# Kernel optimization log

Hardware: AMD Instinct MI355X
Metric: run time of the kernel (lower is better)

The kernel has to match this reference:

```python
import jax, jax.numpy as jnp
import numpy as np

N = 512      # nodes
E = 512      # edges = nb-graph nodes
M = 16384    # nb-graph edges
FIN = 64     # in_node_nf
HID = 128    # hidden_nf
D = 32       # VTV_coord_nf (positional-encoding width)


def _silu(v):
    return v * jax.nn.sigmoid(v)


def _mlp(v, w1, b1, w2, b2):
    # 2-layer MLP with SiLU (matches MLP(in, out, [hidden]))
    return _silu(v @ w1 + b1) @ w2 + b2


def setup_inputs() -> dict:
    key = jax.random.key(0)
    ks = jax.random.split(key, 32)

    def lin(k, i, o, scale=None):
        s = (1.0 / np.sqrt(i)) if scale is None else scale
        return jax.random.normal(k, (i, o), dtype=jnp.float32) * jnp.float32(s)

    inp = {}
    inp['h'] = jax.random.normal(ks[0], (N, FIN), dtype=jnp.float32)
    inp['x'] = jax.random.normal(ks[1], (N, 3), dtype=jnp.float32)
    inp['edges'] = jax.random.randint(ks[2], (2, E), 0, N)
    inp['nb_edge'] = jax.random.randint(ks[3], (2, M), 0, E)
    inp['edge_attr'] = jax.random.normal(ks[4], (E, 4), dtype=jnp.float32)
    inp['nb_num_nodes'] = E  # python int (static)
    # edge_encoder: MLP(2*FIN -> HID -> FIN)
    inp['ew1'] = lin(ks[5], 2 * FIN, HID); inp['eb1'] = jnp.zeros((HID,), jnp.float32)
    inp['ew2'] = lin(ks[6], HID, FIN);     inp['eb2'] = jnp.zeros((FIN,), jnp.float32)
    # PPGN mlp1 / mlp2: MLP(D+FIN -> HID -> FIN)
    inp['p1w1'] = lin(ks[7], D + FIN, HID); inp['p1b1'] = jnp.zeros((HID,), jnp.float32)
    inp['p1w2'] = lin(ks[8], HID, FIN);     inp['p1b2'] = jnp.zeros((FIN,), jnp.float32)
    inp['p2w1'] = lin(ks[9], D + FIN, HID); inp['p2b1'] = jnp.zeros((HID,), jnp.float32)
    inp['p2w2'] = lin(ks[10], HID, FIN);    inp['p2b2'] = jnp.zeros((FIN,), jnp.float32)
    # PPGN output mlp: MLP(D+FIN+FIN -> HID -> FIN) on concat(skip, matmul)
    inp['p3w1'] = lin(ks[11], D + 2 * FIN, HID); inp['p3b1'] = jnp.zeros((HID,), jnp.float32)
    inp['p3w2'] = lin(ks[12], HID, FIN);         inp['p3b2'] = jnp.zeros((FIN,), jnp.float32)
    # IGN 2->1: linear over 5 basis ops
    inp['ign_w'] = lin(ks[13], 5 * FIN, FIN); inp['ign_b'] = jnp.zeros((FIN,), jnp.float32)
    # coord_mlp: Linear(FIN,HID), SiLU, Linear(HID,1,bias=False) with tiny init
    inp['cw1'] = lin(ks[14], FIN, HID); inp['cb1'] = jnp.zeros((HID,), jnp.float32)
    inp['cw2'] = lin(ks[15], HID, 1, scale=0.001)
    # node_dec: MLP(FIN -> HID -> FIN)
    inp['ndw1'] = lin(ks[16], FIN, HID); inp['ndb1'] = jnp.zeros((HID,), jnp.float32)
    inp['ndw2'] = lin(ks[17], HID, FIN); inp['ndb2'] = jnp.zeros((FIN,), jnp.float32)
    return inp


def reference(h, x, edges, nb_edge, edge_attr, nb_num_nodes,
              ew1, eb1, ew2, eb2,
              p1w1, p1b1, p1w2, p1b2,
              p2w1, p2b1, p2w2, p2b2,
              p3w1, p3b1, p3w2, p3b2,
              ign_w, ign_b,
              cw1, cb1, cw2,
              ndw1, ndb1, ndw2, ndb2):
    rows, cols = edges[0], edges[1]
    coord_diff = x[rows] - x[cols]                      # [E,3]
    nbr, nbc = nb_edge[0], nb_edge[1]
    # VTV: inner product of the two relative-position vectors of paired edges
    vtv = jnp.sum(coord_diff[nbr] * coord_diff[nbc], axis=-1)   # [M]
    # sinusoidal positional encoding, a_scale = D/2
    half = D // 2
    div_term = jnp.exp(jnp.log(jnp.float32(10000.0)) * (2.0 * jnp.arange(half, dtype=jnp.float32) / D))
    ang = vtv[:, None] * jnp.float32(D / 2) / div_term          # [M, D/2]
    pe = jnp.stack([jnp.sin(ang), jnp.cos(ang)], axis=-1).reshape(vtv.shape[0], D)
    # node-pair features per original edge
    efn = _mlp(jnp.concatenate([h[rows], h[cols]], axis=1), ew1, eb1, ew2, eb2)  # [E,FIN]
    nb_feat = jnp.concatenate([pe, efn[nbr] * efn[nbc]], axis=1)                 # [M, D+FIN]
    # densify nb-graph 2-tensor and run PPGN block
    En = nb_num_nodes
    T = jnp.zeros((En, En, nb_feat.shape[1]), dtype=nb_feat.dtype).at[nbr, nbc].add(nb_feat)
    m1 = _mlp(T, p1w1, p1b1, p1w2, p1b2)                 # [En,En,FIN]
    m2 = _mlp(T, p2w1, p2b1, p2w2, p2b2)
    mult = jnp.einsum('ikf,kjf->ijf', m1, m2)            # feature-wise matmul
    Tout = _mlp(jnp.concatenate([T, mult], axis=-1), p3w1, p3b1, p3w2, p3b2)
    # IGN 2->1: diag, row-sum, col-sum, total-sum, trace (broadcast)
    idx = jnp.arange(En)
    diag = Tout[idx, idx]                                # [En,FIN]
    rowsum = Tout.sum(axis=1)
    colsum = Tout.sum(axis=0)
    tot = jnp.broadcast_to(Tout.sum(axis=(0, 1)), diag.shape)
    tr = jnp.broadcast_to(diag.sum(axis=0), diag.shape)
    nb_t1 = jnp.concatenate([diag, rowsum, colsum, tot, tr], axis=1) @ ign_w + ign_b  # [En,FIN]
    # coord update: weighted coord_diff, segment-mean over source node
    w = _silu(nb_t1 @ cw1 + cb1) @ cw2                   # [E,1]
    trans = coord_diff * w
    Nn = x.shape[0]
    seg = jax.ops.segment_sum(trans, rows, num_segments=Nn)
    cnt = jax.ops.segment_sum(jnp.ones((rows.shape[0], 1), trans.dtype), rows, num_segments=Nn)
    x_new = x + seg / jnp.clip(cnt, 1.0)
    # node update: scatter_add edge features then residual MLP
    nb_t0 = jax.ops.segment_sum(nb_t1, rows, num_segments=Nn)
    h_new = h + _mlp(nb_t0, ndw1, ndb1, ndw2, ndb2)
    return (h_new, x_new, edge_attr)
```

## Files before the change

### kernel.cpp

```cpp
#include <hip/hip_runtime.h>
#include <hip/hip_bf16.h>

#define NN   512
#define EE   512
#define MM   16384

typedef float v4f __attribute__((ext_vector_type(4)));
typedef short short8v __attribute__((ext_vector_type(8)));

__device__ __forceinline__ float silu_f(float v) { return v / (1.0f + __expf(-v)); }
__device__ __forceinline__ float silu_fast(float v) {
  return v * __builtin_amdgcn_rcpf(1.0f + __expf(-v));
}

__global__ __launch_bounds__(128) void k_front(
    const float* __restrict__ h, const float* __restrict__ x,
    const int* __restrict__ edges, const int* __restrict__ nb_edge,
    const float* __restrict__ ew1, const float* __restrict__ eb1,
    const float* __restrict__ ew2, const float* __restrict__ eb2,
    const float* __restrict__ p1b1, const float* __restrict__ p1w2, const float* __restrict__ p1b2,
    const float* __restrict__ p2b1, const float* __restrict__ p2w2, const float* __restrict__ p2b2,
    const float* __restrict__ p3w1,
    float* __restrict__ coord_diff, float* __restrict__ efn,
    float* __restrict__ c1, float* __restrict__ c2,
    __hip_bfloat16* __restrict__ Wt, int* __restrict__ slotmap) {
  __shared__ float sm[256];
  int b = blockIdx.x, t = threadIdx.x;
  if (b < 512) {
    int r = edges[b], c = edges[EE + b];
    if (t < 3) coord_diff[b * 3 + t] = x[r * 3 + t] - x[c * 3 + t];
    if (t < 64) { sm[t] = h[r * 64 + t]; sm[64 + t] = h[c * 64 + t]; }
    __syncthreads();
    float acc = eb1[t];
    for (int k = 0; k < 128; ++k) acc += sm[k] * ew1[k * 128 + t];
    sm[128 + t] = silu_f(acc);
    __syncthreads();
    if (t < 64) {
      float o = eb2[t];
      for (int k = 0; k < 128; ++k) o += sm[128 + k] * ew2[k * 64 + t];
      efn[b * 64 + t] = o;
    }
  } else if (b == 512) {
    sm[t] = silu_f(p1b1[t]); sm[128 + t] = silu_f(p2b1[t]);
    __syncthreads();
    if (t < 64) {
      float a1 = p1b2[t], a2 = p2b2[t];
      for (int k = 0; k < 128; ++k) { a1 += sm[k] * p1w2[k * 64 + t]; a2 += sm[128 + k] * p2w2[k * 64 + t]; }
      c1[t] = a1; c2[t] = a2;
    }
  } else if (b < 577) {
    int e = (b - 513) * 128 + t;
    int hh = e >> 6, f = e & 63;
    Wt[hh * 64 + f] = __float2bfloat16(p3w1[(96 + f) * 128 + hh]);
  } else {
    int m = (b - 577) * 128 + t;
    int cell = nb_edge[m] * 512 + nb_edge[MM + m];
    atomicCAS(&slotmap[cell], -1, -2);
  }
}

__global__ __launch_bounds__(256) void k_compact(int* __restrict__ slotmap,
                                                 int* __restrict__ slotmapT,
                                                 int* __restrict__ cells,
                                                 int* __restrict__ nC) {
  int cell = blockIdx.x * 256 + threadIdx.x;
  if (slotmap[cell] != -2) return;
  int s = atomicAdd(nC, 1);
  slotmap[cell] = s;
  slotmapT[(cell & 511) * 512 + (cell >> 9)] = s;
  cells[s] = cell;
}

__global__ __launch_bounds__(192) void k_scatterT(
    const int* __restrict__ nb_edge, const int* __restrict__ slotmap,
    const float* __restrict__ coord_diff, const float* __restrict__ efn,
    float* __restrict__ Tc) {
  int t = threadIdx.x;
  int sub = (t >= 96) ? 1 : 0;
  int c = t - sub * 96;
  int m = blockIdx.x * 2 + sub;
  int a = nb_edge[m], b = nb_edge[MM + m];
  int s = slotmap[a * 512 + b];
  float val;
  if (c < 32) {
    float vtv = coord_diff[a * 3 + 0] * coord_diff[b * 3 + 0]
              + coord_diff[a * 3 + 1] * coord_diff[b * 3 + 1]
              + coord_diff[a * 3 + 2] * coord_diff[b * 3 + 2];
    int i = c >> 1;
    float ang = vtv * 16.0f * __expf(-0.57564627324851143f * (float)i);
    val = (c & 1) ? cosf(ang) : sinf(ang);
  } else {
    int f = c - 32;
    val = efn[a * 64 + f] * efn[b * 64 + f];
  }
  atomicAdd(&Tc[s * 96 + c], val);
}

__global__ __launch_bounds__(128) void k_mlp96b(
    const int* __restrict__ cells, const int* __restrict__ nC, const float* __restrict__ Tc,
    const float* __restrict__ w11, const float* __restrict__ b11,
    const float* __restrict__ w12, const float* __restrict__ b12,
    const float* __restrict__ w21, const float* __restrict__ b21,
    const float* __restrict__ w22, const float* __restrict__ b22,
    const float* __restrict__ c1, const float* __restrict__ c2,
    const float* __restrict__ p3w1,
    __hip_bfloat16* __restrict__ Dc1, __hip_bfloat16* __restrict__ Dc2,
    float* __restrict__ A, float* __restrict__ B,
    float* __restrict__ TWc) {
  __shared__ float xsT[96 * 16];
  __shared__ float hid[16][128];
  __shared__ int cl[16];
  int t = threadIdx.x;
  int nc = *nC;
  int s0 = blockIdx.x * 16;
  if (s0 >= nc) return;
  for (int e = t; e < 1536; e += 128) xsT[(e % 96) * 16 + e / 96] = Tc[s0 * 96 + e];
  if (t < 16) cl[t] = (s0 + t < nc) ? cells[s0 + t] : 0;
  __syncthreads();
  float tw[16], a1[16], a2[16];
#pragma unroll
  for (int c = 0; c < 16; ++c) { tw[c] = 0.f; a1[c] = b11[t]; a2[c] = b21[t]; }
  for (int k = 0; k < 96; ++k) {
    float wt = p3w1[k * 128 + t];
    float w1v = w11[k * 128 + t];
    float w2v = w21[k * 128 + t];
    const float4* xr = (const float4*)&xsT[k * 16];
    float4 x0 = xr[0], x1 = xr[1], x2 = xr[2], x3 = xr[3];
    float xv[16] = {x0.x, x0.y, x0.z, x0.w, x1.x, x1.y, x1.z, x1.w,
                    x2.x, x2.y, x2.z, x2.w, x3.x, x3.y, x3.z, x3.w};
#pragma unroll
    for (int c = 0; c < 16; ++c) {
      tw[c] += xv[c] * wt; a1[c] += xv[c] * w1v; a2[c] += xv[c] * w2v;
    }
  }
#pragma unroll
  for (int c = 0; c < 16; ++c) {
    if (s0 + c < nc) TWc[(s0 + c) * 128 + t] = tw[c];
    hid[c][t] = silu_f(a1[c]);
  }
  __syncthreads();
  {
    int hh = t & 63, cq = t >> 6;
    float o[8];
#pragma unroll
    for (int cc = 0; cc < 8; ++cc) o[cc] = b12[hh];
    for (int k = 0; k < 128; ++k) {
      float w = w12[k * 64 + hh];
#pragma unroll
      for (int cc = 0; cc < 8; ++cc) o[cc] += hid[cq * 8 + cc][k] * w;
    }
#pragma unroll
    for (int cc = 0; cc < 8; ++cc) {
      int c = cq * 8 + cc;
      if (s0 + c < nc) {
        float d = o[cc] - c1[hh];
        int cell = cl[c];
        int ai = cell >> 9;
        atomicAdd(&A[ai * 64 + hh], d);
        Dc1[(s0 + c) * 64 + hh] = __float2bfloat16(d);
      }
    }
  }
  __syncthreads();
#pragma unroll
  for (int c = 0; c < 16; ++c) hid[c][t] = silu_f(a2[c]);
  __syncthreads();
  {
    int hh = t & 63, cq = t >> 6;
    float o[8];
#pragma unroll
    for (int cc = 0; cc < 8; ++cc) o[cc] = b22[hh];
    for (int k = 0; k < 128; ++k) {
      float w = w22[k * 64 + hh];
#pragma unroll
      for (int cc = 0; cc < 8; ++cc) o[cc] += hid[cq * 8 + cc][k] * w;
    }
#pragma unroll
    for (int cc = 0; cc < 8; ++cc) {
      int c = cq * 8 + cc;
      if (s0 + c < nc) {
        float d = o[cc] - c2[hh];
        int cell = cl[c];
        int bj = cell & 511;
        atomicAdd(&B[bj * 64 + hh], d);
        Dc2[(s0 + c) * 64 + hh] = __float2bfloat16(d);
      }
    }
  }
}

__global__ __launch_bounds__(128) void k_densify(
    const int* __restrict__ slotmap, const int* __restrict__ slotmapT,
    const __hip_bfloat16* __restrict__ Dc1, const __hip_bfloat16* __restrict__ Dc2,
    __hip_bfloat16* __restrict__ D1d, __hip_bfloat16* __restrict__ D2dT) {
  int b = blockIdx.x;
  int f = b >> 9, row = b & 511;
  int t = threadIdx.x;
  int which = blockIdx.y;
  const int* sm = which ? &slotmapT[row * 512] : &slotmap[row * 512];
  const unsigned short* Dc = (const unsigned short*)(which ? Dc2 : Dc1);
  unsigned short* dst = (unsigned short*)(which ? &D2dT[(f * 512 + row) * 512]
                                                : &D1d[(f * 512 + row) * 512]);
  int4 s4 = *(const int4*)&sm[t * 4];
  ushort4 o;
  o.x = (s4.x >= 0) ? Dc[s4.x * 64 + f] : 0;
  o.y = (s4.y >= 0) ? Dc[s4.y * 64 + f] : 0;
  o.z = (s4.z >= 0) ? Dc[s4.z * 64 + f] : 0;
  o.w = (s4.w >= 0) ? Dc[s4.w * 64 + f] : 0;
  *(ushort4*)&dst[t * 4] = o;
}

__global__ __launch_bounds__(128) void k_uv(
    const float* __restrict__ A, const float* __restrict__ B,
    const float* __restrict__ c1, const float* __restrict__ c2,
    const float* __restrict__ p3w1, const float* __restrict__ p3b1,
    float* __restrict__ u, float* __restrict__ v) {
  __shared__ float vec[64];
  int i = blockIdx.x, y = blockIdx.y, t = threadIdx.x;
  if (t < 64)
    vec[t] = (y == 0) ? (512.0f * c1[t] * c2[t] + c2[t] * A[i * 64 + t])
                      : (c1[t] * B[i * 64 + t]);
  __syncthreads();
  float a = (y == 0) ? p3b1[t] : 0.f;
  for (int f = 0; f < 64; ++f) a += vec[f] * p3w1[(96 + f) * 128 + t];
  (y == 0 ? u : v)[i * 128 + t] = a;
}

__global__ __launch_bounds__(256) void k_einsum_mfma(
    const __hip_bfloat16* __restrict__ D1d,
    const __hip_bfloat16* __restrict__ D2dT,
    __hip_bfloat16* __restrict__ S_fij) {
  __shared__ short As[128 * 40];
  __shared__ short Bs[128 * 40];
  int b = blockIdx.x;
  int f = b >> 4;
  int i0 = ((b >> 2) & 3) * 128, j0 = (b & 3) * 128;
  int t = threadIdx.x;
  int w = t >> 6, lane = t & 63;
  int wy = w >> 1, wx = w & 1;
  int q = lane >> 4, l15 = lane & 15;
  const short* Ap = (const short*)D1d + f * 262144;
  const short* Bp = (const short*)D2dT + f * 262144;
  int row = t >> 1, seg = t & 1;
  v4f acc[4][4];
#pragma unroll
  for (int yi = 0; yi < 4; ++yi)
#pragma unroll
    for (int xj = 0; xj < 4; ++xj) acc[yi][xj] = (v4f){0.f, 0.f, 0.f, 0.f};
  for (int k0 = 0; k0 < 512; k0 += 32) {
    __syncthreads();
    const short8v* ga = (const short8v*)&Ap[(i0 + row) * 512 + k0 + seg * 16];
    const short8v* gb = (const short8v*)&Bp[(j0 + row) * 512 + k0 + seg * 16];
    *(short8v*)&As[row * 40 + seg * 16] = ga[0];
    *(short8v*)&As[row * 40 + seg * 16 + 8] = ga[1];
    *(short8v*)&Bs[row * 40 + seg * 16] = gb[0];
    *(short8v*)&Bs[row * 40 + seg * 16 + 8] = gb[1];
    __syncthreads();
    short8v af[4], bf[4];
#pragma unroll
    for (int x = 0; x < 4; ++x) {
      af[x] = *(const short8v*)&As[(wy * 64 + x * 16 + l15) * 40 + q * 8];
      bf[x] = *(const short8v*)&Bs[(wx * 64 + x * 16 + l15) * 40 + q * 8];
    }
#pragma unroll
    for (int yi = 0; yi < 4; ++yi)
#pragma unroll
      for (int xj = 0; xj < 4; ++xj)
        acc[yi][xj] = __builtin_amdgcn_mfma_f32_16x16x32_bf16(af[yi], bf[xj], acc[yi][xj], 0, 0, 0);
  }
#pragma unroll
  for (int yi = 0; yi < 4; ++yi)
#pragma unroll
    for (int r = 0; r < 4; ++r) {
      int irow = i0 + wy * 64 + yi * 16 + q * 4 + r;
#pragma unroll
      for (int xj = 0; xj < 4; ++xj)
        S_fij[(f * 512 + irow) * 512 + j0 + wx * 64 + xj * 16 + l15] =
            __float2bfloat16(acc[yi][xj][r]);
    }
}

__global__ __launch_bounds__(256) void k_transpose(
    const __hip_bfloat16* __restrict__ S_fij, __hip_bfloat16* __restrict__ S) {
  __shared__ short lds[64 * 72];
  int t = threadIdx.x;
  int ij0 = blockIdx.x * 64;
  const short* src = (const short*)S_fij;
#pragma unroll
  for (int p = 0; p < 2; ++p) {
    int f = p * 32 + (t >> 3), seg = t & 7;
    short8v ga = *(const short8v*)&src[f * 262144 + ij0 + seg * 8];
    int fgrp = f >> 3, flo = f & 7;
#pragma unroll
    for (int k = 0; k < 8; ++k) {
      int ij = seg * 8 + k;
      int swz = (fgrp ^ (ij & 7) ^ ((ij >> 3) & 7)) & 7;
      lds[ij * 72 + swz * 8 + flo] = ga[k];
    }
  }
  __syncthreads();
  short* dst = (short*)S;
#pragma unroll
  for (int p = 0; p < 2; ++p) {
    int ij = p * 32 + (t >> 3), fseg = t & 7;
    int swz = (fseg ^ (ij & 7) ^ ((ij >> 3) & 7)) & 7;
    short8v val = *(const short8v*)&lds[ij * 72 + swz * 8];
    *(short8v*)&dst[(ij0 + ij) * 64 + fseg * 8] = val;
  }
}

__global__ __launch_bounds__(256) void k_tout_mfma(
    const __hip_bfloat16* __restrict__ S, const float* __restrict__ u,
    const float* __restrict__ v, const __hip_bfloat16* __restrict__ Wt,
    float* __restrict__ row_part, float* __restrict__ col_part,
    float* __restrict__ diag_silu) {
  __shared__ __hip_bfloat16 WtL[128 * 72];
  __shared__ __hip_bfloat16 uvL[4096];
  __shared__ __hip_bfloat16 colbuf[4][16][140];
  int t = threadIdx.x;
  int w = t >> 6, lane = t & 63;
  int q = lane >> 4, l15 = lane & 15;
  int bi = blockIdx.x >> 5, bj = blockIdx.x & 31;
  int i0 = bi * 16, j0 = bj * 16;
  for (int e = t; e < 4096; e += 256) {
    int row = e >> 5, c2 = e & 31;
    ((unsigned*)WtL)[row * 36 + c2] = ((const unsigned*)Wt)[row * 32 + c2];
  }
  for (int e = t; e < 2048; e += 256)
    uvL[e] = __float2bfloat16(u[(i0 + (e >> 7)) * 128 + (e & 127)]);
  for (int e = t; e < 2048; e += 256)
    uvL[2048 + e] = __float2bfloat16(v[(j0 + (e >> 7)) * 128 + (e & 127)]);
  short8v a[4][2];
#pragma unroll
  for (int mt = 0; mt < 4; ++mt) {
    const short8v* sp =
        (const short8v*)&S[((i0 + w * 4 + mt) * 512 + j0 + l15) * 64];
    a[mt][0] = sp[q];
    a[mt][1] = sp[4 + q];
  }
  __syncthreads();
#pragma unroll
  for (int half = 0; half < 2; ++half) {
    v4f acc[4][4];
#pragma unroll
    for (int mt = 0; mt < 4; ++mt)
#pragma unroll
      for (int n4 = 0; n4 < 4; ++n4) {
        int nt = half * 4 + n4;
        const short8v* b0 = (const short8v*)&WtL[(nt * 16 + l15) * 72 + q * 8];
        const short8v* b1 = (const short8v*)&WtL[(nt * 16 + l15) * 72 + 32 + q * 8];
        v4f c = {0.f, 0.f, 0.f, 0.f};
        c = __builtin_amdgcn_mfma_f32_16x16x32_bf16(a[mt][0], *b0, c, 0, 0, 0);
        c = __builtin_amdgcn_mfma_f32_16x16x32_bf16(a[mt][1], *b1, c, 0, 0, 0);
        acc[mt][n4] = c;
      }
#pragma unroll
    for (int n4 = 0; n4 < 4; ++n4) {
      int nt = half * 4 + n4;
      int hh = nt * 16 + l15;
      float uu[4];
#pragma unroll
      for (int mt = 0; mt < 4; ++mt)
        uu[mt] = __bfloat162float(uvL[(w * 4 + mt) * 128 + hh]);
      float rs[4] = {0.f, 0.f, 0.f, 0.f};
#pragma unroll
      for (int r = 0; r < 4; ++r) {
        int jL = q * 4 + r;
        float cs = 0.f;
        float vv = __bfloat162float(uvL[2048 + jL * 128 + hh]);
#pragma unroll
        for (int mt = 0; mt < 4; ++mt) {
          int iL = w * 4 + mt;
          float sv = silu_fast(acc[mt][n4][r] + uu[mt] + vv);
          rs[mt] += sv;
          cs += sv;
          if (bi == bj && iL == jL) diag_silu[(i0 + iL) * 128 + hh] = sv;
        }
        colbuf[w][jL][hh] = __float2bfloat16(cs);
      }
#pragma unroll
      for (int mt = 0; mt < 4; ++mt) {
        float rsum = rs[mt];
        rsum += __shfl_xor(rsum, 16);
        rsum += __shfl_xor(rsum, 32);
        if (q == 0)
          row_part[(bj * 512 + i0 + w * 4 + mt) * 128 + hh] = rsum;
      }
    }
  }
  __syncthreads();
  for (int e = t; e < 2048; e += 256) {
    int jL = e >> 7, hh = e & 127;
    float acc4 = __bfloat162float(colbuf[0][jL][hh]) + __bfloat162float(colbuf[1][jL][hh]) +
                 __bfloat162float(colbuf[2][jL][hh]) + __bfloat162float(colbuf[3][jL][hh]);
    col_part[(bi * 512 + j0 + jL) * 128 + hh] = acc4;
  }
}

__global__ __launch_bounds__(128) void k_corr(
    const int* __restrict__ cells, const int* __restrict__ nC,
    const __hip_bfloat16* __restrict__ S, const float* __restrict__ u,
    const float* __restrict__ v, const float* __restrict__ TWc,
    const __hip_bfloat16* __restrict__ Wt,
    float* __restrict__ corr_row, float* __restrict__ corr_col,
    float* __restrict__ diag_silu) {
  __shared__ float sf[64];
  int s = blockIdx.x;
  if (s >= *nC) return;
  int t = threadIdx.x;
  int cell = cells[s];
  int ai = cell >> 9, bj = cell & 511;
  if (t < 64) sf[t] = __bfloat162float(S[(ai * 512 + bj) * 64 + t]);
  __syncthreads();
  float acc = 0.f;
  const __hip_bfloat16* wr = &Wt[t * 64];
  for (int f = 0; f < 64; ++f) acc += sf[f] * __bfloat162float(wr[f]);
  float z0 = acc + u[ai * 128 + t] + v[bj * 128 + t];
  float zc = z0 + TWc[s * 128 + t];
  float d = silu_fast(zc) - silu_fast(z0);
  atomicAdd(&corr_row[ai * 128 + t], d);
  atomicAdd(&corr_col[bj * 128 + t], d);
  if (ai == bj) atomicAdd(&diag_silu[ai * 128 + t], d);
}

__global__ __launch_bounds__(128) void k_tout2f(
    const float* __restrict__ diag_silu, const float* __restrict__ row_part,
    const float* __restrict__ col_part,
    const float* __restrict__ corr_row, const float* __restrict__ corr_col,
    const float* __restrict__ w2, const float* __restrict__ b2,
    float* __restrict__ diag_T, float* __restrict__ row_T, float* __restrict__ col_T,
    float* __restrict__ tot, float* __restrict__ tr) {
  __shared__ float in[128];
  int e = blockIdx.x, which = blockIdx.y, t = threadIdx.x;
  float a;
  if (which == 0) {
    a = diag_silu[e * 128 + t];
  } else {
    const float* src = (which == 1) ? row_part : col_part;
    a = (which == 1) ? corr_row[e * 128 + t] : corr_col[e * 128 + t];
    for (int p = 0; p < 32; ++p) a += src[(p * 512 + e) * 128 + t];
  }
  in[t] = a;
  __syncthreads();
  if (t < 64) {
    float o = 0.f;
    for (int k = 0; k < 128; ++k) o += in[k] * w2[k * 64 + t];
    float val = o + b2[t] * ((which == 0) ? 1.0f : 512.0f);
    if (which == 0)      { diag_T[e * 64 + t] = val; atomicAdd(&tr[t], val); }
    else if (which == 1) { row_T[e * 64 + t] = val; atomicAdd(&tot[t], val); }
    else                 { col_T[e * 64 + t] = val; }
  }
}

__global__ __launch_bounds__(128) void k_nbt1_edge(
    const float* __restrict__ diag_T, const float* __restrict__ row_T,
    const float* __restrict__ col_T, const float* __restrict__ tot,
    const float* __restrict__ tr,
    const float* __restrict__ gw, const float* __restrict__ gb,
    const int* __restrict__ edges, const float* __restrict__ coord_diff,
    const float* __restrict__ edge_attr,
    const float* __restrict__ cw1, const float* __restrict__ cb1,
    const float* __restrict__ cw2,
    float* __restrict__ seg, float* __restrict__ cnt, float* __restrict__ nb_t0,
    float* __restrict__ out_ea) {
  __shared__ float in[320];
  __shared__ float nbt[64];
  __shared__ float red[128];
  int e = blockIdx.x, t = threadIdx.x;
  if (t < 64) {
    in[t] = diag_T[e * 64 + t]; in[64 + t] = row_T[e * 64 + t];
    in[128 + t] = col_T[e * 64 + t]; in[192 + t] = tot[t]; in[256 + t] = tr[t];
  }
  __syncthreads();
  if (t < 64) {
    float a = gb[t];
    for (int k = 0; k < 320; ++k) a += in[k] * gw[k * 64 + t];
    nbt[t] = a;
  }
  __syncthreads();
  float a = cb1[t];
  for (int k = 0; k < 64; ++k) a += nbt[k] * cw1[k * 128 + t];
  red[t] = silu_f(a) * cw2[t];
  __syncthreads();
  for (int s2 = 64; s2 > 0; s2 >>= 1) {
    if (t < s2) red[t] += red[t + s2];
    __syncthreads();
  }
  float w = red[0];
  int r = edges[e];
  if (t < 3) atomicAdd(&seg[r * 3 + t], coord_diff[e * 3 + t] * w);
  if (t == 64) atomicAdd(&cnt[r], 1.0f);
  if (t < 64) atomicAdd(&nb_t0[r * 64 + t], nbt[t]);
  if (t < 4) out_ea[e * 4 + t] = edge_attr[e * 4 + t];
}

__global__ __launch_bounds__(128) void k_node_out(
    const float* __restrict__ h, const float* __restrict__ x,
    const float* __restrict__ seg, const float* __restrict__ cnt,
    const float* __restrict__ nb_t0,
    const float* __restrict__ w1, const float* __restrict__ b1,
    const float* __restrict__ w2, const float* __restrict__ b2,
    float* __restrict__ out_h, float* __restrict__ out_x) {
  __shared__ float in[64];
  __shared__ float hs[128];
  int n = blockIdx.x, t = threadIdx.x;
  if (t < 3) {
    float c = cnt[n]; if (c < 1.f) c = 1.f;
    out_x[n * 3 + t] = x[n * 3 + t] + seg[n * 3 + t] / c;
  }
  if (t < 64) in[t] = nb_t0[n * 64 + t];
  __syncthreads();
  float a = b1[t];
  for (int k = 0; k < 64; ++k) a += in[k] * w1[k * 128 + t];
  hs[t] = silu_f(a);
  __syncthreads();
  if (t < 64) {
    float o = b2[t];
    for (int k = 0; k < 128; ++k) o += hs[k] * w2[k * 64 + t];
    out_h[n * 64 + t] = h[n * 64 + t] + o;
  }
}

extern "C" void kernel_launch(void* const* d_in, const int* in_sizes, int n_in,
                              void* d_out, int out_size, void* d_ws, size_t ws_size,
                              hipStream_t stream) {
  (void)in_sizes; (void)n_in; (void)out_size; (void)ws_size;
  const float* h  = (const float*)d_in[0];
  const float* x  = (const float*)d_in[1];
  const int* edges   = (const int*)d_in[2];
  const int* nb_edge = (const int*)d_in[3];
  const float* edge_attr = (const float*)d_in[4];
  const float* ew1 = (const float*)d_in[6],  *eb1 = (const float*)d_in[7];
  const float* ew2 = (const float*)d_in[8],  *eb2 = (const float*)d_in[9];
  const float* p1w1 = (const float*)d_in[10], *p1b1 = (const float*)d_in[11];
  const float* p1w2 = (const float*)d_in[12], *p1b2 = (const float*)d_in[13];
  const float* p2w1 = (const float*)d_in[14], *p2b1 = (const float*)d_in[15];
  const float* p2w2 = (const float*)d_in[16], *p2b2 = (const float*)d_in[17];
  const float* p3w1 = (const float*)d_in[18], *p3b1 = (const float*)d_in[19];
  const float* p3w2 = (const float*)d_in[20], *p3b2 = (const float*)d_in[21];
  const float* ignw = (const float*)d_in[22], *ignb = (const float*)d_in[23];
  const float* cw1 = (const float*)d_in[24], *cb1 = (const float*)d_in[25];
  const float* cw2 = (const float*)d_in[26];
  const float* ndw1 = (const float*)d_in[27], *ndb1 = (const float*)d_in[28];
  const float* ndw2 = (const float*)d_in[29], *ndb2 = (const float*)d_in[30];

  char* ws = (char*)d_ws;
  __hip_bfloat16* D1d  = (__hip_bfloat16*)(ws + 0);
  __hip_bfloat16* S    = (__hip_bfloat16*)(ws + 0);
  __hip_bfloat16* D2dT = (__hip_bfloat16*)(ws + 33554432);
  __hip_bfloat16* S_fij = (__hip_bfloat16*)(ws + 67108864);
  float* row_part = (float*)(ws + 100663296);
  float* col_part = (float*)(ws + 117440512);
  float* Tc    = (float*)(ws + 134217728);
  int*   nC    = (int*)(ws + 140509184);
  float* A     = (float*)(ws + 140509200);
  float* B     = (float*)(ws + 140640272);
  float* seg   = (float*)(ws + 140771344);
  float* cnt   = (float*)(ws + 140777488);
  float* nb_t0 = (float*)(ws + 140779536);
  float* tot   = (float*)(ws + 140910608);
  float* tr    = (float*)(ws + 140910864);
  float* corr_row = (float*)(ws + 140911120);
  float* corr_col = (float*)(ws + 141173264);
  int*   slotmap  = (int*)(ws + 141435904);
  int*   slotmapT = (int*)(ws + 142484480);
  int*   cells    = (int*)(ws + 143533056);
  __hip_bfloat16* Dc1 = (__hip_bfloat16*)(ws + 143598592);
  __hip_bfloat16* Dc2 = (__hip_bfloat16*)(ws + 145695744);
  float* TWc      = (float*)(ws + 147792896);
  float* c1       = (float*)(ws + 156181504);
  float* c2       = (float*)(ws + 156181760);
  float* u        = (float*)(ws + 156182016);
  float* v        = (float*)(ws + 156444160);
  float* coord_diff  = (float*)(ws + 156706304);
  float* efn         = (float*)(ws + 156712448);
  float* diag_silu   = (float*)(ws + 156843520);
  float* diag_T      = (float*)(ws + 157105664);
  float* row_T       = (float*)(ws + 157236736);
  float* col_T       = (float*)(ws + 157367808);
  __hip_bfloat16* Wt  = (__hip_bfloat16*)(ws + 157629952);

  float* out_h  = (float*)d_out;
  float* out_x  = out_h + 512 * 64;
  float* out_ea = out_x + 512 * 3;

  hipMemsetAsync(slotmap, 0xFF, 2097152, stream);
  hipMemsetAsync(ws + 134217728, 0, 7217680, stream);

  k_front<<<705, 128, 0, stream>>>(h, x, edges, nb_edge,
                                   ew1, eb1, ew2, eb2,
                                   p1b1, p1w2, p1b2, p2b1, p2w2, p2b2, p3w1,
                                   coord_diff, efn, c1, c2, Wt, slotmap);
  k_compact<<<1024, 256, 0, stream>>>(slotmap, slotmapT, cells, nC);
  k_scatterT<<<8192, 192, 0, stream>>>(nb_edge, slotmap, coord_diff, efn, Tc);
  k_mlp96b<<<1024, 128, 0, stream>>>(cells, nC, Tc,
                                     p1w1, p1b1, p1w2, p1b2,
                                     p2w1, p2b1, p2w2, p2b2,
                                     c1, c2, p3w1, Dc1, Dc2, A, B, TWc);
  k_densify<<<dim3(32768, 2), 128, 0, stream>>>(slotmap, slotmapT, Dc1, Dc2,
                                                D1d, D2dT);
  k_uv<<<dim3(512, 2), 128, 0, stream>>>(A, B, c1, c2, p3w1, p3b1, u, v);
  k_einsum_mfma<<<1024, 256, 0, stream>>>(D1d, D2dT, S_fij);
  k_transpose<<<4096, 256, 0, stream>>>(S_fij, S);
  k_tout_mfma<<<1024, 256, 0, stream>>>(S, u, v, Wt,
                                        row_part, col_part, diag_silu);
  k_corr<<<16384, 128, 0, stream>>>(cells, nC, S, u, v, TWc, Wt,
                                    corr_row, corr_col, diag_silu);
  k_tout2f<<<dim3(512, 3), 128, 0, stream>>>(diag_silu, row_part, col_part,
                                             corr_row, corr_col,
                                             p3w2, p3b2, diag_T, row_T, col_T,
                                             tot, tr);
  k_nbt1_edge<<<512, 128, 0, stream>>>(diag_T, row_T, col_T, tot, tr,
                                       ignw, ignb, edges, coord_diff, edge_attr,
                                       cw1, cb1, cw2, seg, cnt, nb_t0, out_ea);
  k_node_out<<<512, 128, 0, stream>>>(h, x, seg, cnt, nb_t0,
                                      ndw1, ndb1, ndw2, ndb2, out_h, out_x);
}
```

Baseline: 420.0 us.

## Replace scalar per-cell MLP kernel with bf16 MFMA GEMM kernels

The fused fp32 scalar kernel computing the cell MLPs is split into three kernels. The first converts Tc and the weights to bf16, transposing the weights. The second runs a 128x384x96 bf16 MFMA GEMM producing TWc and the SiLU hidden activations. The third runs a second MFMA GEMM with the bias and centering subtraction, the atomics and the Dc outputs. This moves the dense MLP work onto matrix cores, at the cost of bf16 rounding on the inputs, weights and hidden activations, two extra launches and intermediate H1/H2 buffers in global memory.

```diff
diff --git a/kernel.cpp b/kernel.cpp
--- a/kernel.cpp
+++ b/kernel.cpp
@@ -96,97 +96,160 @@
   atomicAdd(&Tc[s * 96 + c], val);
 }
 
-__global__ __launch_bounds__(128) void k_mlp96b(
-    const int* __restrict__ cells, const int* __restrict__ nC, const float* __restrict__ Tc,
-    const float* __restrict__ w11, const float* __restrict__ b11,
-    const float* __restrict__ w12, const float* __restrict__ b12,
-    const float* __restrict__ w21, const float* __restrict__ b21,
-    const float* __restrict__ w22, const float* __restrict__ b22,
+__global__ __launch_bounds__(256) void k_prep2(
+    const float* __restrict__ Tc,
+    const float* __restrict__ p3w1, const float* __restrict__ w11,
+    const float* __restrict__ w21, const float* __restrict__ w12,
+    const float* __restrict__ w22,
+    __hip_bfloat16* __restrict__ TcB, __hip_bfloat16* __restrict__ WBT,
+    __hip_bfloat16* __restrict__ W2T) {
+  int i = blockIdx.x * 256 + threadIdx.x;
+  if (i < 16384 * 96) { TcB[i] = __float2bfloat16(Tc[i]); return; }
+  i -= 16384 * 96;
+  if (i < 384 * 96) {
+    int n = i / 96, k = i % 96;
+    float v = (n < 128) ? p3w1[k * 128 + n]
+            : (n < 256) ? w11[k * 128 + (n - 128)]
+                        : w21[k * 128 + (n - 256)];
+    WBT[i] = __float2bfloat16(v);
+    return;
+  }
+  i -= 384 * 96;
+  {
+    int which = i >> 13, rem = i & 8191;
+    int n = rem >> 7, k = rem & 127;
+    const float* w2 = which ? w22 : w12;
+    W2T[i] = __float2bfloat16(w2[k * 64 + n]);
+  }
+}
+
+__global__ __launch_bounds__(256) void k_gemm1(
+    const int* __restrict__ nC, const __hip_bfloat16* __restrict__ TcB,
+    const __hip_bfloat16* __restrict__ WBT,
+    const float* __restrict__ b11, const float* __restrict__ b21,
+    float* __restrict__ TWc, __hip_bfloat16* __restrict__ H1,
+    __hip_bfloat16* __restrict__ H2) {
+  __shared__ short As[128 * 104];
+  __shared__ short Bs[128 * 104];
+  int i0 = blockIdx.x * 128;
+  int nt = blockIdx.y;
+  if (i0 >= *nC) return;
+  int t = threadIdx.x;
+  int w = t >> 6, lane = t & 63;
+  int wy = w >> 1, wx = w & 1;
+  int q = lane >> 4, l15 = lane & 15;
+  const short* Ap = (const short*)TcB;
+  const short* Bp = (const short*)WBT + nt * 128 * 96;
+  for (int idx = t; idx < 1536; idx += 256) {
+    int row = idx / 12, seg = idx % 12;
+    *(short8v*)&As[row * 104 + seg * 8] = *(const short8v*)&Ap[(i0 + row) * 96 + seg * 8];
+    *(short8v*)&Bs[row * 104 + seg * 8] = *(const short8v*)&Bp[row * 96 + seg * 8];
+  }
+  __syncthreads();
+  v4f acc[4][4];
+#pragma unroll
+  for (int yi = 0; yi < 4; ++yi)
+#pragma unroll
+    for (int xj = 0; xj < 4; ++xj) acc[yi][xj] = (v4f){0.f, 0.f, 0.f, 0.f};
+#pragma unroll
+  for (int k0 = 0; k0 < 96; k0 += 32) {
+    short8v af[4], bf[4];
+#pragma unroll
+    for (int x = 0; x < 4; ++x) {
+      af[x] = *(const short8v*)&As[(wy * 64 + x * 16 + l15) * 104 + k0 + q * 8];
+      bf[x] = *(const short8v*)&Bs[(wx * 64 + x * 16 + l15) * 104 + k0 + q * 8];
+    }
+#pragma unroll
+    for (int yi = 0; yi < 4; ++yi)
+#pragma unroll
+      for (int xj = 0; xj < 4; ++xj)
+        acc[yi][xj] = __builtin_amdgcn_mfma_f32_16x16x32_bf16(af[yi], bf[xj], acc[yi][xj], 0, 0, 0);
+  }
+#pragma unroll
+  for (int yi = 0; yi < 4; ++yi)
+#pragma unroll
+    for (int r = 0; r < 4; ++r) {
+      int s = i0 + wy * 64 + yi * 16 + q * 4 + r;
+#pragma unroll
+      for (int xj = 0; xj < 4; ++xj) {
+        int j = wx * 64 + xj * 16 + l15;
+        float val = acc[yi][xj][r];
+        if (nt == 0) TWc[s * 128 + j] = val;
+        else if (nt == 1) H1[s * 128 + j] = __float2bfloat16(silu_f(val + b11[j]));
+        else H2[s * 128 + j] = __float2bfloat16(silu_f(val + b21[j]));
+      }
+    }
+}
+
+__global__ __launch_bounds__(256) void k_gemm2(
+    const int* __restrict__ nC, const int* __restrict__ cells,
+    const __hip_bfloat16* __restrict__ H1, const __hip_bfloat16* __restrict__ H2,
+    const __hip_bfloat16* __restrict__ W2T,
+    const float* __restrict__ b12, const float* __restrict__ b22,
     const float* __restrict__ c1, const float* __restrict__ c2,
-    const float* __restrict__ p3w1,
     __hip_bfloat16* __restrict__ Dc1, __hip_bfloat16* __restrict__ Dc2,
-    float* __restrict__ A, float* __restrict__ B,
-    float* __restrict__ TWc) {
-  __shared__ float xsT[96 * 16];
-  __shared__ float hid[16][128];
-  __shared__ int cl[16];
-  int t = threadIdx.x;
+    float* __restrict__ A, float* __restrict__ B) {
+  __shared__ short Hs[128 * 136];
+  __shared__ short Wsh[64 * 136];
+  __shared__ int cellL[128];
+  int i0 = blockIdx.x * 128;
+  int which = blockIdx.y;
   int nc = *nC;
-  int s0 = blockIdx.x * 16;
-  if (s0 >= nc) return;
-  for (int e = t; e < 1536; e += 128) xsT[(e % 96) * 16 + e / 96] = Tc[s0 * 96 + e];
-  if (t < 16) cl[t] = (s0 + t < nc) ? cells[s0 + t] : 0;
-  __syncthreads();
-  float tw[16], a1[16], a2[16];
-#pragma unroll
-  for (int c = 0; c < 16; ++c) { tw[c] = 0.f; a1[c] = b11[t]; a2[c] = b21[t]; }
-  for (int k = 0; k < 96; ++k) {
-    float wt = p3w1[k * 128 + t];
-    float w1v = w11[k * 128 + t];
-    float w2v = w21[k * 128 + t];
-    const float4* xr = (const float4*)&xsT[k * 16];
-    float4 x0 = xr[0], x1 = xr[1], x2 = xr[2], x3 = xr[3];
-    float xv[16] = {x0.x, x0.y, x0.z, x0.w, x1.x, x1.y, x1.z, x1.w,
-                    x2.x, x2.y, x2.z, x2.w, x3.x, x3.y, x3.z, x3.w};
-#pragma unroll
-    for (int c = 0; c < 16; ++c) {
-      tw[c] += xv[c] * wt; a1[c] += xv[c] * w1v; a2[c] += xv[c] * w2v;
-    }
-  }
-#pragma unroll
-  for (int c = 0; c < 16; ++c) {
-    if (s0 + c < nc) TWc[(s0 + c) * 128 + t] = tw[c];
-    hid[c][t] = silu_f(a1[c]);
-  }
-  __syncthreads();
-  {
-    int hh = t & 63, cq = t >> 6;
-    float o[8];
-#pragma unroll
-    for (int cc = 0; cc < 8; ++cc) o[cc] = b12[hh];
-    for (int k = 0; k < 128; ++k) {
-      float w = w12[k * 64 + hh];
-#pragma unroll
-      for (int cc = 0; cc < 8; ++cc) o[cc] += hid[cq * 8 + cc][k] * w;
-    }
-#pragma unroll
-    for (int cc = 0; cc < 8; ++cc) {
-      int c = cq * 8 + cc;
-      if (s0 + c < nc) {
-        float d = o[cc] - c1[hh];
-        int cell = cl[c];
-        int ai = cell >> 9;
-        atomicAdd(&A[ai * 64 + hh], d);
-        Dc1[(s0 + c) * 64 + hh] = __float2bfloat16(d);
+  if (i0 >= nc) return;
+  int t = threadIdx.x;
+  int w = t >> 6, lane = t & 63;
+  int q = lane >> 4, l15 = lane & 15;
+  const short* Hp = (const short*)(which ? H2 : H1);
+  const short* Wp = (const short*)W2T + which * 64 * 128;
+  for (int idx = t; idx < 2048; idx += 256) {
+    int row = idx >> 4, seg = idx & 15;
+    *(short8v*)&Hs[row * 136 + seg * 8] = *(const short8v*)&Hp[(i0 + row) * 128 + seg * 8];
+  }
+  for (int idx = t; idx < 1024; idx += 256) {
+    int row = idx >> 4, seg = idx & 15;
+    *(short8v*)&Wsh[row * 136 + seg * 8] = *(const short8v*)&Wp[row * 128 + seg * 8];
+  }
+  if (t < 128) cellL[t] = (i0 + t < nc) ? cells[i0 + t] : 0;
+  __syncthreads();
+  v4f acc[2][4];
+#pragma unroll
+  for (int y = 0; y < 2; ++y)
+#pragma unroll
+    for (int xj = 0; xj < 4; ++xj) acc[y][xj] = (v4f){0.f, 0.f, 0.f, 0.f};
+#pragma unroll
+  for (int k0 = 0; k0 < 128; k0 += 32) {
+    short8v af[2], bf[4];
+#pragma unroll
+    for (int y = 0; y < 2; ++y)
+      af[y] = *(const short8v*)&Hs[(w * 32 + y * 16 + l15) * 136 + k0 + q * 8];
+#pragma unroll
+    for (int xj = 0; xj < 4; ++xj)
+      bf[xj] = *(const short8v*)&Wsh[(xj * 16 + l15) * 136 + k0 + q * 8];
+#pragma unroll
+    for (int y = 0; y < 2; ++y)
+#pragma unroll
+      for (int xj = 0; xj < 4; ++xj)
+        acc[y][xj] = __builtin_amdgcn_mfma_f32_16x16x32_bf16(af[y], bf[xj], acc[y][xj], 0, 0, 0);
+  }
+  const float* bias = which ? b22 : b12;
+  const float* cc = which ? c2 : c1;
+#pragma unroll
+  for (int y = 0; y < 2; ++y)
+#pragma unroll
+    for (int r = 0; r < 4; ++r) {
+      int lrow = w * 32 + y * 16 + q * 4 + r;
+      int s = i0 + lrow;
+      if (s >= nc) continue;
+      int cell = cellL[lrow];
+      int idx = which ? (cell & 511) : (cell >> 9);
+#pragma unroll
+      for (int xj = 0; xj < 4; ++xj) {
+        int hh = xj * 16 + l15;
+        float d = acc[y][xj][r] + bias[hh] - cc[hh];
+        if (which) { atomicAdd(&B[idx * 64 + hh], d); Dc2[s * 64 + hh] = __float2bfloat16(d); }
+        else       { atomicAdd(&A[idx * 64 + hh], d); Dc1[s * 64 + hh] = __float2bfloat16(d); }
       }
     }
-  }
-  __syncthreads();
-#pragma unroll
-  for (int c = 0; c < 16; ++c) hid[c][t] = silu_f(a2[c]);
-  __syncthreads();
-  {
-    int hh = t & 63, cq = t >> 6;
-    float o[8];
-#pragma unroll
-    for (int cc = 0; cc < 8; ++cc) o[cc] = b22[hh];
-    for (int k = 0; k < 128; ++k) {
-      float w = w22[k * 64 + hh];
-#pragma unroll
-      for (int cc = 0; cc < 8; ++cc) o[cc] += hid[cq * 8 + cc][k] * w;
-    }
-#pragma unroll
-    for (int cc = 0; cc < 8; ++cc) {
-      int c = cq * 8 + cc;
-      if (s0 + c < nc) {
-        float d = o[cc] - c2[hh];
-        int cell = cl[c];
-        int bj = cell & 511;
-        atomicAdd(&B[bj * 64 + hh], d);
-        Dc2[(s0 + c) * 64 + hh] = __float2bfloat16(d);
-      }
-    }
-  }
 }
 
 __global__ __launch_bounds__(128) void k_densify(
@@ -549,6 +612,11 @@
   __hip_bfloat16* S    = (__hip_bfloat16*)(ws + 0);
   __hip_bfloat16* D2dT = (__hip_bfloat16*)(ws + 33554432);
   __hip_bfloat16* S_fij = (__hip_bfloat16*)(ws + 67108864);
+  __hip_bfloat16* TcB = (__hip_bfloat16*)(ws + 67108864);
+  __hip_bfloat16* H1  = (__hip_bfloat16*)(ws + 70254592);
+  __hip_bfloat16* H2  = (__hip_bfloat16*)(ws + 74448896);
+  __hip_bfloat16* WBT = (__hip_bfloat16*)(ws + 78643200);
+  __hip_bfloat16* W2T = (__hip_bfloat16*)(ws + 78716928);
   float* row_part = (float*)(ws + 100663296);
   float* col_part = (float*)(ws + 117440512);
   float* Tc    = (float*)(ws + 134217728);
@@ -593,10 +661,13 @@
                                    coord_diff, efn, c1, c2, Wt, slotmap);
   k_compact<<<1024, 256, 0, stream>>>(slotmap, slotmapT, cells, nC);
   k_scatterT<<<8192, 192, 0, stream>>>(nb_edge, slotmap, coord_diff, efn, Tc);
-  k_mlp96b<<<1024, 128, 0, stream>>>(cells, nC, Tc,
-                                     p1w1, p1b1, p1w2, p1b2,
-                                     p2w1, p2b1, p2w2, p2b2,
-                                     c1, c2, p3w1, Dc1, Dc2, A, B, TWc);
+  k_prep2<<<6352, 256, 0, stream>>>(Tc, p3w1, p1w1, p2w1, p1w2, p2w2,
+                                    TcB, WBT, W2T);
+  k_gemm1<<<dim3(128, 3), 256, 0, stream>>>(nC, TcB, WBT, p1b1, p2b1,
+                                            TWc, H1, H2);
+  k_gemm2<<<dim3(128, 2), 256, 0, stream>>>(nC, cells, H1, H2, W2T,
+                                            p1b2, p2b2, c1, c2,
+                                            Dc1, Dc2, A, B);
   k_densify<<<dim3(32768, 2), 128, 0, stream>>>(slotmap, slotmapT, Dc1, Dc2,
                                                 D1d, D2dT);
   k_uv<<<dim3(512, 2), 128, 0, stream>>>(A, B, c1, c2, p3w1, p3b1, u, v);
```

New measurement: 409.1 us. 1.03x faster.
